# Kernel tuning notes

Hardware: AMD Instinct MI355X
Metric: run time of the kernel (lower is better)

The kernel has to match this reference:

```python
import jax, jax.numpy as jnp
import numpy as np

IMG = 512
C = 3
PS = 16
G = 32
B = 64
NH = IMG // PS
NW = IMG // PS
NP_ = NH * NW
P2 = PS * PS


def setup_inputs() -> dict:
    key = jax.random.key(0)
    k1, k2, k3, k4 = jax.random.split(key, 4)
    x = jax.random.normal(k1, (B, C, IMG, IMG), dtype=jnp.float32)
    # Conv2d(1, ps*ps, kernel=ps) default init ~ U(-1/ps, 1/ps); scale random normals similarly.
    obfuscation_weights = jax.random.normal(k2, (C, G, P2, P2), dtype=jnp.float32) / PS
    obfuscation_biases = jax.random.normal(k3, (C, G, P2), dtype=jnp.float32) / PS
    channel_permutation = jax.random.permutation(k4, jnp.arange(C, dtype=jnp.int32))
    return {
        "x": x,
        "obfuscation_weights": obfuscation_weights,
        "obfuscation_biases": obfuscation_biases,
        "channel_permutation": channel_permutation,
    }


def reference(x, obfuscation_weights, obfuscation_biases, channel_permutation):
    # x: (B, C, H, W) -> patches (B, C, N, ps*ps)
    x_patched = (
        x.reshape(B, C, NH, PS, NW, PS)
        .transpose(0, 1, 2, 4, 3, 5)
        .reshape(B, C, NP_, P2)
    )
    # group index per spatial patch: (row + col) % group_size
    ridx = jnp.arange(NH)[:, None]
    cidx = jnp.arange(NW)[None, :]
    group_map = ((ridx + cidx) % G).reshape(-1)  # (N,)
    sel_w = obfuscation_weights[:, group_map]  # (C, N, P2, P2)
    sel_b = obfuscation_biases[:, group_map]  # (C, N, P2)
    out = jnp.einsum("bcnp,cnpo->bcno", x_patched, sel_w) + sel_b
    # back to image layout
    out = (
        out.reshape(B, C, NH, NW, PS, PS)
        .transpose(0, 1, 2, 4, 3, 5)
        .reshape(B, C, IMG, IMG)
    )
    out = out[:, channel_permutation]
    return jnp.tanh(out)
```

## Files before the change

kernel.cpp:

```cpp
#include <hip/hip_runtime.h>

#define C_SZ   3
#define IMG_SZ 512

typedef short  short8 __attribute__((ext_vector_type(8)));
typedef float  f32x4  __attribute__((ext_vector_type(4)));
typedef unsigned short u16;
typedef u16    u16x8  __attribute__((ext_vector_type(8)));

__device__ __forceinline__ u16 f2bf(float f) {
    unsigned u = __float_as_uint(f);
    u += 0x7FFFu + ((u >> 16) & 1u);
    return (u16)(u >> 16);
}

__device__ __forceinline__ float tanh_fast(float v) {
    float e = __expf(2.f * v);
    return 1.f - 2.f * __builtin_amdgcn_rcpf(e + 1.f);
}

__device__ __forceinline__ void gload_lds16(const float* g, float* l) {
    __builtin_amdgcn_global_load_lds(
        (const __attribute__((address_space(1))) void*)g,
        (__attribute__((address_space(3))) void*)l, 16, 0, 0);
}

__device__ __forceinline__ short8 gload_b128(const u16* p) {
    short8 d;
    asm volatile("global_load_dwordx4 %0, %1, off"
                 : "=v"(d) : "v"(p) : "memory");
    return d;
}

__global__ __launch_bounds__(256)
void prep_wt(const float* __restrict__ w, u16* __restrict__ wt) {
    const int cg = blockIdx.x;
    const int kb = blockIdx.y;
    __shared__ float T[32][260];
    const int tid = threadIdx.x;
    const float* wb = w + (size_t)cg * 65536 + (size_t)kb * 32 * 256;
    #pragma unroll
    for (int pass = 0; pass < 8; ++pass) {
        int q = pass * 256 + tid;
        int pl = q >> 6, o4 = (q & 63) * 4;
        float4 v = *reinterpret_cast<const float4*>(wb + (size_t)pl * 256 + o4);
        T[pl][o4 + 0] = v.x; T[pl][o4 + 1] = v.y;
        T[pl][o4 + 2] = v.z; T[pl][o4 + 3] = v.w;
    }
    __syncthreads();
    u16* dst = wt + ((size_t)cg * 8 + kb) * 8192;
    #pragma unroll
    for (int h0 = 0; h0 < 4; ++h0) {
        int h = h0 * 256 + tid;
        int kg = h >> 8, n = h & 255;
        u16x8 v;
        #pragma unroll
        for (int e = 0; e < 8; ++e) v[e] = f2bf(T[kg * 8 + e][n]);
        *reinterpret_cast<u16x8*>(dst + (size_t)kg * 2048 + n * 8) = v;
    }
}

__global__ __launch_bounds__(512)
void obf_mfma(const float* __restrict__ x,
              const u16*  __restrict__ wt,
              const float* __restrict__ bias,
              const int*  __restrict__ perm,
              float* __restrict__ out)
{
    const int bid  = blockIdx.x;
    const int xcd  = bid & 7;
    const int i    = bid >> 3;
    const int g    = i & 31;
    const int s    = xcd * 6 + (i >> 5);
    const int c    = s >> 4;
    const int mtile = s & 15;
    const int cg   = c * 32 + g;

    const int tid  = threadIdx.x;
    const int lane = tid & 63, wv = tid >> 6;
    const int wr   = wv >> 2, wc = wv & 3;
    const int r = lane & 15, kg = lane >> 4;

    __shared__ float As[3][4096];

    int cp = 0;
    #pragma unroll
    for (int ii = 0; ii < C_SZ; ++ii) if (perm[ii] == c) cp = ii;

    const float* g_src[2];
    #pragma unroll
    for (int j = 0; j < 2; ++j) {
        int q    = wv * 128 + j * 64 + lane;
        int row  = q >> 3;
        int lpos = (q & 7) ^ (row & 7);
        int mg   = mtile * 128 + row;
        int b    = mg >> 5, nh = mg & 31, nw = (g - nh) & 31;
        g_src[j] = x + (((size_t)(b * C_SZ + c) * IMG_SZ + nh * 16 + (lpos >> 2)) * IMG_SZ
                        + nw * 16 + (lpos & 3) * 4);
    }
    const u16* bsrc = wt + (size_t)cg * 65536 + kg * 2048 + (size_t)(wc * 64 + r) * 8;

    const int p0 = (((2 * kg)     ^ (r & 7)) * 4);
    const int p1 = (((2 * kg + 1) ^ (r & 7)) * 4);
    const int rbase = (wr * 64 + r) * 32;

    f32x4 acc[4][4] = {};
    short8 bv[2][4];

#define STAGE_A(t) do {                                                \
        float* d_ = &As[(t) % 3][0] + wv * 512;                        \
        gload_lds16(g_src[0] + (size_t)(t) * 1024, d_);                \
        gload_lds16(g_src[1] + (size_t)(t) * 1024, d_ + 256);          \
    } while (0)

    STAGE_A(0);
    #pragma unroll
    for (int ni = 0; ni < 4; ++ni)
        bv[0][ni] = gload_b128(bsrc + ni * 128);

    #pragma unroll
    for (int t = 0; t < 8; ++t) {
        if (t < 7) {
            STAGE_A(t + 1);
            #pragma unroll
            for (int ni = 0; ni < 4; ++ni)
                bv[(t + 1) & 1][ni] = gload_b128(bsrc + (t + 1) * 8192 + ni * 128);
            asm volatile("s_waitcnt vmcnt(6)" ::: "memory");
        } else {
            asm volatile("s_waitcnt vmcnt(0)" ::: "memory");
        }
        __builtin_amdgcn_sched_barrier(0);
        __builtin_amdgcn_s_barrier();

        const float* lb = &As[t % 3][0];
        #pragma unroll
        for (int mi = 0; mi < 4; ++mi) {
            f32x4 v0 = *reinterpret_cast<const f32x4*>(lb + (rbase + mi * 16 * 32) + p0);
            f32x4 v1 = *reinterpret_cast<const f32x4*>(lb + (rbase + mi * 16 * 32) + p1);
            short8 af;
            af[0] = (short)f2bf(v0[0]); af[1] = (short)f2bf(v0[1]);
            af[2] = (short)f2bf(v0[2]); af[3] = (short)f2bf(v0[3]);
            af[4] = (short)f2bf(v1[0]); af[5] = (short)f2bf(v1[1]);
            af[6] = (short)f2bf(v1[2]); af[7] = (short)f2bf(v1[3]);
            #pragma unroll
            for (int ni = 0; ni < 4; ++ni)
                acc[mi][ni] = __builtin_amdgcn_mfma_f32_16x16x32_bf16(
                    bv[t & 1][ni], af, acc[mi][ni], 0, 0, 0);
        }
    }
#undef STAGE_A

    const float* bb = bias + (size_t)cg * 256 + wc * 64 + kg * 4;
    float4 bsv[4];
    #pragma unroll
    for (int ni = 0; ni < 4; ++ni)
        bsv[ni] = *reinterpret_cast<const float4*>(bb + ni * 16);

    #pragma unroll
    for (int mi = 0; mi < 4; ++mi) {
        const int mg = mtile * 128 + wr * 64 + mi * 16 + r;
        const int b  = mg >> 5, nh = mg & 31, nw = (g - nh) & 31;
        float* pbase = out + ((size_t)(b * C_SZ + cp) * IMG_SZ + nh * 16) * IMG_SZ
                           + nw * 16 + kg * 4;
        #pragma unroll
        for (int ni = 0; ni < 4; ++ni) {
            const int rp = wc * 4 + ni;
            float4 v;
            v.x = tanh_fast(acc[mi][ni][0] + bsv[ni].x);
            v.y = tanh_fast(acc[mi][ni][1] + bsv[ni].y);
            v.z = tanh_fast(acc[mi][ni][2] + bsv[ni].z);
            v.w = tanh_fast(acc[mi][ni][3] + bsv[ni].w);
            *reinterpret_cast<float4*>(pbase + (size_t)rp * IMG_SZ) = v;
        }
    }
}

extern "C" void kernel_launch(void* const* d_in, const int* in_sizes, int n_in,
                              void* d_out, int out_size, void* d_ws, size_t ws_size,
                              hipStream_t stream) {
    const float* x    = (const float*)d_in[0];
    const float* w    = (const float*)d_in[1];
    const float* bias = (const float*)d_in[2];
    const int*   perm = (const int*)d_in[3];
    float* out = (float*)d_out;
    u16*   wt  = (u16*)d_ws;

    dim3 pgrid(C_SZ * 32, 8, 1);
    prep_wt<<<pgrid, 256, 0, stream>>>(w, wt);

    obf_mfma<<<1536, 512, 0, stream>>>(x, wt, bias, perm, out);
}
```

Measured before the change: 126.2 us.

## Stage weight tiles through LDS with direct global-to-LDS loads

Weight (B operand) fragments are no longer loaded per-wave from global memory into registers. Instead they are cooperatively staged into a double-buffered LDS array with global_load_lds, then read from LDS for the MFMAs. The A buffer drops from triple to double buffering, which requires an extra barrier at the end of each iteration to avoid overwriting live data. The aim is to stop four column-waves from redundantly fetching the same weight data, at the cost of more LDS use, extra LDS reads and added synchronization.

Result: slower. 128.8 us (+2.0%).

```diff
diff --git a/kernel.cpp b/kernel.cpp
--- a/kernel.cpp
+++ b/kernel.cpp
@@ -19,17 +19,10 @@
     return 1.f - 2.f * __builtin_amdgcn_rcpf(e + 1.f);
 }
 
-__device__ __forceinline__ void gload_lds16(const float* g, float* l) {
+__device__ __forceinline__ void gload_lds16(const void* g, void* l) {
     __builtin_amdgcn_global_load_lds(
         (const __attribute__((address_space(1))) void*)g,
         (__attribute__((address_space(3))) void*)l, 16, 0, 0);
-}
-
-__device__ __forceinline__ short8 gload_b128(const u16* p) {
-    short8 d;
-    asm volatile("global_load_dwordx4 %0, %1, off"
-                 : "=v"(d) : "v"(p) : "memory");
-    return d;
 }
 
 __global__ __launch_bounds__(256)
@@ -81,7 +74,8 @@
     const int wr   = wv >> 2, wc = wv & 3;
     const int r = lane & 15, kg = lane >> 4;
 
-    __shared__ float As[3][4096];
+    __shared__ float As[2][4096];
+    __shared__ u16   Bs[2][8192];
 
     int cp = 0;
     #pragma unroll
@@ -98,41 +92,49 @@
         g_src[j] = x + (((size_t)(b * C_SZ + c) * IMG_SZ + nh * 16 + (lpos >> 2)) * IMG_SZ
                         + nw * 16 + (lpos & 3) * 4);
     }
-    const u16* bsrc = wt + (size_t)cg * 65536 + kg * 2048 + (size_t)(wc * 64 + r) * 8;
+    const u16* b_src = wt + (size_t)cg * 65536 + wv * 512 + lane * 8;
 
     const int p0 = (((2 * kg)     ^ (r & 7)) * 4);
     const int p1 = (((2 * kg + 1) ^ (r & 7)) * 4);
     const int rbase = (wr * 64 + r) * 32;
 
     f32x4 acc[4][4] = {};
-    short8 bv[2][4];
 
 #define STAGE_A(t) do {                                                \
-        float* d_ = &As[(t) % 3][0] + wv * 512;                        \
+        float* d_ = &As[(t) & 1][0] + wv * 512;                        \
         gload_lds16(g_src[0] + (size_t)(t) * 1024, d_);                \
         gload_lds16(g_src[1] + (size_t)(t) * 1024, d_ + 256);          \
     } while (0)
+#define STAGE_B(t) do {                                                \
+        u16* bd_ = &Bs[(t) & 1][0] + wv * 512;                         \
+        const u16* bs_ = b_src + (size_t)(t) * 8192;                   \
+        gload_lds16(bs_,        bd_);                                  \
+        gload_lds16(bs_ + 4096, bd_ + 4096);                           \
+    } while (0)
 
     STAGE_A(0);
-    #pragma unroll
-    for (int ni = 0; ni < 4; ++ni)
-        bv[0][ni] = gload_b128(bsrc + ni * 128);
+    STAGE_B(0);
 
     #pragma unroll
     for (int t = 0; t < 8; ++t) {
         if (t < 7) {
             STAGE_A(t + 1);
-            #pragma unroll
-            for (int ni = 0; ni < 4; ++ni)
-                bv[(t + 1) & 1][ni] = gload_b128(bsrc + (t + 1) * 8192 + ni * 128);
-            asm volatile("s_waitcnt vmcnt(6)" ::: "memory");
+            STAGE_B(t + 1);
+            asm volatile("s_waitcnt vmcnt(4)" ::: "memory");
         } else {
             asm volatile("s_waitcnt vmcnt(0)" ::: "memory");
         }
         __builtin_amdgcn_sched_barrier(0);
         __builtin_amdgcn_s_barrier();
 
-        const float* lb = &As[t % 3][0];
+        const float* lb  = &As[t & 1][0];
+        const u16*   lbB = &Bs[t & 1][0];
+        short8 bf[4];
+        #pragma unroll
+        for (int ni = 0; ni < 4; ++ni)
+            bf[ni] = *reinterpret_cast<const short8*>(
+                lbB + kg * 2048 + (wc * 64 + ni * 16 + r) * 8);
+
         #pragma unroll
         for (int mi = 0; mi < 4; ++mi) {
             f32x4 v0 = *reinterpret_cast<const f32x4*>(lb + (rbase + mi * 16 * 32) + p0);
@@ -145,10 +147,12 @@
             #pragma unroll
             for (int ni = 0; ni < 4; ++ni)
                 acc[mi][ni] = __builtin_amdgcn_mfma_f32_16x16x32_bf16(
-                    bv[t & 1][ni], af, acc[mi][ni], 0, 0, 0);
+                    bf[ni], af, acc[mi][ni], 0, 0, 0);
         }
+        if (t < 7) __builtin_amdgcn_s_barrier();
     }
 #undef STAGE_A
+#undef STAGE_B
 
     const float* bb = bias + (size_t)cg * 256 + wc * 64 + kg * 4;
     float4 bsv[4];
```
